# Kernel tuning notes

Hardware: AMD Instinct MI355X
Metric: run time of the kernel (lower is better)

The kernel has to match this reference:

```python
import jax, jax.numpy as jnp
import numpy as np

K = 499  # kernel_size


def setup_inputs() -> dict:
    key = jax.random.key(0)
    k1, k2 = jax.random.split(key)
    B, F, T = 32, 64, 8000
    # nonnegative spectrogram input, shape (B, 1, F, T)
    x = jax.random.uniform(k1, (B, 1, F, T), dtype=jnp.float32)
    a = 0.90 + 0.099 * jax.random.uniform(k2, (F,), dtype=jnp.float32)
    w = jnp.ones((F,), dtype=jnp.float32)
    return {"x": x, "a": a, "w": w}


def _build_kernel(a, w, dtype):
    # powers[f, k] = a_f ** k, k = 0..K-2
    F = a.shape[0]
    powers = a[:, None] ** jnp.arange(K - 1, dtype=dtype)  # (F, K-1)
    C = 1.0 / powers.sum(axis=1)                            # (F,)
    neg = (-C * w)[:, None] * powers                        # (F, K-1)
    # pre-flip kernel = [1, neg_0, ..., neg_{K-2}]; flipped -> [neg_{K-2}, ..., neg_0, 1]
    kern = jnp.concatenate([neg[:, ::-1], jnp.ones((F, 1), dtype)], axis=1)  # (F, K)
    return kern[:, None, :]  # (F, 1, K) OIH, groups = F


def reference(x, a, w):
    dtype = x.dtype
    kern = _build_kernel(a.astype(dtype), w.astype(dtype), dtype)
    xs = x[:, 0]  # (B, F, T)
    # replicate (edge) pad on the left by K-1 along time
    xp = jnp.pad(xs, ((0, 0), (0, 0), (K - 1, 0)), mode="edge")
    y = jax.lax.conv_general_dilated(
        xp, kern,
        window_strides=(1,), padding="VALID",
        dimension_numbers=("NCH", "OIH", "NCH"),
        feature_group_count=xs.shape[1],
    )  # (B, F, T)
    return jnp.abs(y)[:, None]  # (B, 1, F, T)
```

## Files before the change

kernel.cpp:

```cpp
#include <hip/hip_runtime.h>
#include <math.h>


constexpr int T      = 8000;
constexpr int F      = 64;
constexpr int B      = 32;
constexpr int KM1    = 498;
constexpr int NSEG   = 4;
constexpr int SEGLEN = T / NSEG;
constexpr int ROUND  = 512;
constexpr int NFULL  = SEGLEN / ROUND;
constexpr int TAILN  = SEGLEN - NFULL * ROUND;

#define DPP_F(x, ctrl, rm) \
  __builtin_bit_cast(float, __builtin_amdgcn_update_dpp(0, __builtin_bit_cast(int, (x)), (ctrl), (rm), 0xf, false))

__device__ __forceinline__ double dpow(double b, int e) {
    double r = 1.0, p = b;
    while (e) { if (e & 1) r *= p; p *= p; e >>= 1; }
    return r;
}

__global__ __launch_bounds__(256) void willmore_scan_kernel(
    const float* __restrict__ x, const float* __restrict__ a,
    const float* __restrict__ w, float* __restrict__ out)
{
    const int row  = blockIdx.x;
    const int seg  = threadIdx.x >> 6;
    const int lane = threadIdx.x & 63;
    const int f = row % F;

    const float* xr   = x   + (size_t)row * T;
    float*       orow = out + (size_t)row * T;

    const double ad     = (double)a[f];
    const double a498d  = dpow(ad, KM1);
    const double sumgeo = (1.0 - a498d) / (1.0 - ad);
    const double r_d    = dpow(ad, 8);
    const float  af     = (float)ad;
    const float  na498  = (float)(-a498d);
    const float  g      = (float)(1.0 / sumgeo) * w[f];
    const float  r1     = (float)r_d;
    const float  r2     = (float)(r_d * r_d);
    const float  r4     = (float)dpow(r_d, 4);
    const float  r8     = (float)dpow(r_d, 8);
    const float  a512   = (float)dpow(r_d, 64);
    const float  inv_r  = (float)(1.0 / r_d);
    const float  alane  = (float)dpow(r_d, lane);
    const float  wA     = (float)dpow(r_d, (lane & 15) + 1);
    const float  wB     = (float)dpow(r_d, (lane & 31) + 1);

    const int t0 = seg * SEGLEN;

    float S;
    if (t0 == 0) {
        S = xr[0] * (float)sumgeo;
    } else {
        const int base = t0 - 512 + 8 * lane;
        const float4 v0 = *(const float4*)(xr + base);
        const float4 v1 = *(const float4*)(xr + base + 4);
        float xs[8] = {v0.x, v0.y, v0.z, v0.w, v1.x, v1.y, v1.z, v1.w};
        #pragma unroll
        for (int i = 0; i < 8; ++i) { if (511 - 8 * lane - i >= KM1) xs[i] = 0.0f; }
        float h = xs[0];
        #pragma unroll
        for (int i = 1; i < 8; ++i) h = fmaf(h, af, xs[i]);
        float contrib = (float)dpow(ad, 504 - 8 * lane) * h;
        #pragma unroll
        for (int s = 1; s < 64; s <<= 1) contrib += __shfl_xor(contrib, s, 64);
        S = contrib;
    }

    #pragma unroll
    for (int rnd = 0; rnd <= NFULL; ++rnd) {
        const bool last = (rnd == NFULL);
        const int tR = t0 + rnd * ROUND;
        int tb = tR + 8 * lane;
        if (last) tb = min(tb, T - 8);

        const float4 v0 = *(const float4*)(xr + tb);
        const float4 v1 = *(const float4*)(xr + tb + 4);
        const float xv[8] = {v0.x, v0.y, v0.z, v0.w, v1.x, v1.y, v1.z, v1.w};

        const int lg = tb - KM1;
        float lv[8];
        if (t0 == 0 && rnd == 0) {
            #pragma unroll
            for (int i = 0; i < 8; ++i) lv[i] = xr[max(lg + i, 0)];
        } else {
            const float2 p0 = *(const float2*)(xr + lg);
            const float2 p1 = *(const float2*)(xr + lg + 2);
            const float2 p2 = *(const float2*)(xr + lg + 4);
            const float2 p3 = *(const float2*)(xr + lg + 6);
            lv[0]=p0.x; lv[1]=p0.y; lv[2]=p1.x; lv[3]=p1.y;
            lv[4]=p2.x; lv[5]=p2.y; lv[6]=p3.x; lv[7]=p3.y;
        }

        float u[8];
        #pragma unroll
        for (int i = 0; i < 8; ++i) u[i] = fmaf(na498, lv[i], xv[i]);

        float q = u[0];
        #pragma unroll
        for (int i = 1; i < 8; ++i) q = fmaf(q, af, u[i]);

        float G = q;
        G = fmaf(r1, DPP_F(G, 0x111, 0xf), G);
        G = fmaf(r2, DPP_F(G, 0x112, 0xf), G);
        G = fmaf(r4, DPP_F(G, 0x114, 0xf), G);
        G = fmaf(r8, DPP_F(G, 0x118, 0xf), G);
        G = fmaf(wA, DPP_F(G, 0x142, 0xa), G);
        G = fmaf(wB, DPP_F(G, 0x143, 0xc), G);

        const float E = (G - q) * inv_r;

        float s = fmaf(alane, S, E);
        float y[8];
        #pragma unroll
        for (int i = 0; i < 8; ++i) {
            y[i] = fabsf(fmaf(-g, s, xv[i]));
            s = fmaf(af, s, u[i]);
        }

        if (!last || lane < TAILN / 8) {
            *(float4*)(orow + tb)     = make_float4(y[0], y[1], y[2], y[3]);
            *(float4*)(orow + tb + 4) = make_float4(y[4], y[5], y[6], y[7]);
        }

        if (!last) {
            const float G63 = __builtin_bit_cast(float,
                __builtin_amdgcn_readlane(__builtin_bit_cast(int, G), 63));
            S = fmaf(a512, S, G63);
        }
    }
}

extern "C" void kernel_launch(void* const* d_in, const int* in_sizes, int n_in,
                              void* d_out, int out_size, void* d_ws, size_t ws_size,
                              hipStream_t stream) {
    const float* x = (const float*)d_in[0];
    const float* a = (const float*)d_in[1];
    const float* w = (const float*)d_in[2];
    float* out = (float*)d_out;

    const int blocks = B * F;
    hipLaunchKernelGGL(willmore_scan_kernel, dim3(blocks), dim3(256), 0, stream,
                       x, a, w, out);
}
```

Before: 123.6 us.

## Give each wavefront one independent 512-sample chunk instead of serial rounds

Each wavefront now handles a single 512-sample chunk of a row. It rebuilds the carry-in state from the preceding window with a shuffle reduction, so no cross-round serial dependency is needed. The grid grows from one block per row to 16 chunks per row, four waves per block. This removes the serial round loop and raises parallelism, at the cost of redundant window loads and reductions per chunk. It also replaces the double-precision power loops for per-lane weights with float exponentiation by squaring, which may cost accuracy for powers near 1.

```diff
diff --git a/kernel.cpp b/kernel.cpp
--- a/kernel.cpp
+++ b/kernel.cpp
@@ -2,15 +2,12 @@
 #include <math.h>
 
 
-constexpr int T      = 8000;
-constexpr int F      = 64;
-constexpr int B      = 32;
-constexpr int KM1    = 498;
-constexpr int NSEG   = 4;
-constexpr int SEGLEN = T / NSEG;
-constexpr int ROUND  = 512;
-constexpr int NFULL  = SEGLEN / ROUND;
-constexpr int TAILN  = SEGLEN - NFULL * ROUND;
+constexpr int T     = 8000;
+constexpr int F     = 64;
+constexpr int B     = 32;
+constexpr int KM1   = 498;
+constexpr int CHUNK = 512;
+constexpr int CPR   = (T + CHUNK - 1) / CHUNK;
 
 #define DPP_F(x, ctrl, rm) \
   __builtin_bit_cast(float, __builtin_amdgcn_update_dpp(0, __builtin_bit_cast(int, (x)), (ctrl), (rm), 0xf, false))
@@ -21,14 +18,22 @@
     return r;
 }
 
+__device__ __forceinline__ float powi(float base, int e) {
+    float r = 1.0f, p = base;
+    #pragma unroll
+    for (int b = 0; b < 9; ++b) { r = (e & (1 << b)) ? r * p : r; p *= p; }
+    return r;
+}
+
 __global__ __launch_bounds__(256) void willmore_scan_kernel(
     const float* __restrict__ x, const float* __restrict__ a,
     const float* __restrict__ w, float* __restrict__ out)
 {
-    const int row  = blockIdx.x;
-    const int seg  = threadIdx.x >> 6;
-    const int lane = threadIdx.x & 63;
-    const int f = row % F;
+    const int wid   = blockIdx.x * 4 + (threadIdx.x >> 6);
+    const int lane  = threadIdx.x & 63;
+    const int row   = wid >> 4;
+    const int chunk = wid & (CPR - 1);
+    const int f     = row % F;
 
     const float* xr   = x   + (size_t)row * T;
     float*       orow = out + (size_t)row * T;
@@ -44,94 +49,84 @@
     const float  r2     = (float)(r_d * r_d);
     const float  r4     = (float)dpow(r_d, 4);
     const float  r8     = (float)dpow(r_d, 8);
-    const float  a512   = (float)dpow(r_d, 64);
     const float  inv_r  = (float)(1.0 / r_d);
-    const float  alane  = (float)dpow(r_d, lane);
-    const float  wA     = (float)dpow(r_d, (lane & 15) + 1);
-    const float  wB     = (float)dpow(r_d, (lane & 31) + 1);
+    const float  alane  = powi(af, 8 * lane);
+    const float  wA     = powi(af, 8 * ((lane & 15) + 1));
+    const float  wB     = powi(af, 8 * ((lane & 31) + 1));
 
-    const int t0 = seg * SEGLEN;
+    const int t0   = chunk * CHUNK;
+    const int tb_u = t0 + 8 * lane;
+    const int tb   = min(tb_u, T - 8);
+
+    const float4 m0 = *(const float4*)(xr + tb);
+    const float4 m1 = *(const float4*)(xr + tb + 4);
+
+    float ws8[8];
+    float lv[8];
+    const int lg = tb - KM1;
+    if (chunk > 0) {
+        const int wb = t0 - CHUNK + 8 * lane;
+        const float4 w0 = *(const float4*)(xr + wb);
+        const float4 w1 = *(const float4*)(xr + wb + 4);
+        ws8[0]=w0.x; ws8[1]=w0.y; ws8[2]=w0.z; ws8[3]=w0.w;
+        ws8[4]=w1.x; ws8[5]=w1.y; ws8[6]=w1.z; ws8[7]=w1.w;
+        const float2 p0 = *(const float2*)(xr + lg);
+        const float2 p1 = *(const float2*)(xr + lg + 2);
+        const float2 p2 = *(const float2*)(xr + lg + 4);
+        const float2 p3 = *(const float2*)(xr + lg + 6);
+        lv[0]=p0.x; lv[1]=p0.y; lv[2]=p1.x; lv[3]=p1.y;
+        lv[4]=p2.x; lv[5]=p2.y; lv[6]=p3.x; lv[7]=p3.y;
+    } else {
+        #pragma unroll
+        for (int i = 0; i < 8; ++i) lv[i] = xr[max(lg + i, 0)];
+    }
 
     float S;
-    if (t0 == 0) {
+    if (chunk == 0) {
+        S = m0.x;
         S = xr[0] * (float)sumgeo;
     } else {
-        const int base = t0 - 512 + 8 * lane;
-        const float4 v0 = *(const float4*)(xr + base);
-        const float4 v1 = *(const float4*)(xr + base + 4);
-        float xs[8] = {v0.x, v0.y, v0.z, v0.w, v1.x, v1.y, v1.z, v1.w};
         #pragma unroll
-        for (int i = 0; i < 8; ++i) { if (511 - 8 * lane - i >= KM1) xs[i] = 0.0f; }
-        float h = xs[0];
+        for (int i = 0; i < 8; ++i) { if (8 * lane + i < 14) ws8[i] = 0.0f; }
+        float h = ws8[0];
         #pragma unroll
-        for (int i = 1; i < 8; ++i) h = fmaf(h, af, xs[i]);
-        float contrib = (float)dpow(ad, 504 - 8 * lane) * h;
+        for (int i = 1; i < 8; ++i) h = fmaf(h, af, ws8[i]);
+        float contrib = powi(af, 504 - 8 * lane) * h;
         #pragma unroll
         for (int s = 1; s < 64; s <<= 1) contrib += __shfl_xor(contrib, s, 64);
         S = contrib;
     }
 
+    const float xv[8] = {m0.x, m0.y, m0.z, m0.w, m1.x, m1.y, m1.z, m1.w};
+    float u[8];
     #pragma unroll
-    for (int rnd = 0; rnd <= NFULL; ++rnd) {
-        const bool last = (rnd == NFULL);
-        const int tR = t0 + rnd * ROUND;
-        int tb = tR + 8 * lane;
-        if (last) tb = min(tb, T - 8);
+    for (int i = 0; i < 8; ++i) u[i] = fmaf(na498, lv[i], xv[i]);
 
-        const float4 v0 = *(const float4*)(xr + tb);
-        const float4 v1 = *(const float4*)(xr + tb + 4);
-        const float xv[8] = {v0.x, v0.y, v0.z, v0.w, v1.x, v1.y, v1.z, v1.w};
+    float q = u[0];
+    #pragma unroll
+    for (int i = 1; i < 8; ++i) q = fmaf(q, af, u[i]);
 
-        const int lg = tb - KM1;
-        float lv[8];
-        if (t0 == 0 && rnd == 0) {
-            #pragma unroll
-            for (int i = 0; i < 8; ++i) lv[i] = xr[max(lg + i, 0)];
-        } else {
-            const float2 p0 = *(const float2*)(xr + lg);
-            const float2 p1 = *(const float2*)(xr + lg + 2);
-            const float2 p2 = *(const float2*)(xr + lg + 4);
-            const float2 p3 = *(const float2*)(xr + lg + 6);
-            lv[0]=p0.x; lv[1]=p0.y; lv[2]=p1.x; lv[3]=p1.y;
-            lv[4]=p2.x; lv[5]=p2.y; lv[6]=p3.x; lv[7]=p3.y;
-        }
+    float G = q;
+    G = fmaf(r1, DPP_F(G, 0x111, 0xf), G);
+    G = fmaf(r2, DPP_F(G, 0x112, 0xf), G);
+    G = fmaf(r4, DPP_F(G, 0x114, 0xf), G);
+    G = fmaf(r8, DPP_F(G, 0x118, 0xf), G);
+    G = fmaf(wA, DPP_F(G, 0x142, 0xa), G);
+    G = fmaf(wB, DPP_F(G, 0x143, 0xc), G);
 
-        float u[8];
-        #pragma unroll
-        for (int i = 0; i < 8; ++i) u[i] = fmaf(na498, lv[i], xv[i]);
+    const float E = (G - q) * inv_r;
 
-        float q = u[0];
-        #pragma unroll
-        for (int i = 1; i < 8; ++i) q = fmaf(q, af, u[i]);
+    float s = fmaf(alane, S, E);
+    float y[8];
+    #pragma unroll
+    for (int i = 0; i < 8; ++i) {
+        y[i] = fabsf(fmaf(-g, s, xv[i]));
+        s = fmaf(af, s, u[i]);
+    }
 
-        float G = q;
-        G = fmaf(r1, DPP_F(G, 0x111, 0xf), G);
-        G = fmaf(r2, DPP_F(G, 0x112, 0xf), G);
-        G = fmaf(r4, DPP_F(G, 0x114, 0xf), G);
-        G = fmaf(r8, DPP_F(G, 0x118, 0xf), G);
-        G = fmaf(wA, DPP_F(G, 0x142, 0xa), G);
-        G = fmaf(wB, DPP_F(G, 0x143, 0xc), G);
-
-        const float E = (G - q) * inv_r;
-
-        float s = fmaf(alane, S, E);
-        float y[8];
-        #pragma unroll
-        for (int i = 0; i < 8; ++i) {
-            y[i] = fabsf(fmaf(-g, s, xv[i]));
-            s = fmaf(af, s, u[i]);
-        }
-
-        if (!last || lane < TAILN / 8) {
-            *(float4*)(orow + tb)     = make_float4(y[0], y[1], y[2], y[3]);
-            *(float4*)(orow + tb + 4) = make_float4(y[4], y[5], y[6], y[7]);
-        }
-
-        if (!last) {
-            const float G63 = __builtin_bit_cast(float,
-                __builtin_amdgcn_readlane(__builtin_bit_cast(int, G), 63));
-            S = fmaf(a512, S, G63);
-        }
+    if (tb_u <= T - 8) {
+        *(float4*)(orow + tb)     = make_float4(y[0], y[1], y[2], y[3]);
+        *(float4*)(orow + tb + 4) = make_float4(y[4], y[5], y[6], y[7]);
     }
 }
 
@@ -143,7 +138,7 @@
     const float* w = (const float*)d_in[2];
     float* out = (float*)d_out;
 
-    const int blocks = B * F;
+    const int blocks = B * F * CPR / 4;
     hipLaunchKernelGGL(willmore_scan_kernel, dim3(blocks), dim3(256), 0, stream,
                        x, a, w, out);
 }
```

Result: faster. 116.0 us (-6.2%).
